# Kernel tuning notes

Measured on AMD Instinct MI355X. Metric: run time of the kernel, lower is better.

## Reference

```python
import jax, jax.numpy as jnp
import numpy as np

EPS_BN = 1e-5
EPS_W = 1e-16
UP_CH = [512, 256, 128, 64]
NS = [512, 2048, 8192, 32768]
K = 3


def knn_interpolate(x, pos, pos_up, batch, batch_up, k):
    # squared distances [N_up, N]; cross-batch pairs masked to +inf
    d = jnp.sum((pos_up[:, None, :] - pos[None, :, :]) ** 2, axis=-1)
    d = jnp.where(batch_up[:, None] != batch[None, :], jnp.inf, d)
    neg_d, idx = jax.lax.top_k(-d, k)             # k nearest neighbours
    w = 1.0 / jnp.maximum(-neg_d, EPS_W)          # inverse squared-distance weights
    xn = x[idx]                                   # [N_up, k, C] gather
    return jnp.einsum('nk,nkc->nc', w, xn) / jnp.sum(w, axis=1, keepdims=True)


def lin_bn_relu(h, W, b, g, be):
    # Linear -> BatchNorm (batch stats over nodes) -> ReLU (PyG MLP, plain_last=False)
    h = h @ W.T + b
    m = jnp.mean(h, axis=0)
    v = jnp.var(h, axis=0)
    return jax.nn.relu((h - m) * jax.lax.rsqrt(v + EPS_BN) * g + be)


def decoder_fwd(pos, x, batch, params):
    x_i = x[0]
    for i in range(3):  # fixed num_convs=3 levels, structurally distinct shapes
        up = knn_interpolate(x_i, pos[i], pos[i + 1], batch[i], batch[i + 1], K)
        h = jnp.concatenate([x[i + 1], up], axis=-1)
        W1, b1, g1, be1, W2, b2, g2, be2 = params[i]
        h = lin_bn_relu(h, W1, b1, g1, be1)            # MLP block
        x_i = h + lin_bn_relu(h, W2, b2, g2, be2)      # ResMLP residual block
    return x_i


def setup_inputs() -> dict:
    key = jax.random.key(0)
    ks = jax.random.split(key, 32)
    inp = {}
    for i, (n, c) in enumerate(zip(NS, UP_CH)):
        inp[f'pos{i}'] = jax.random.normal(ks[i], (n, 3), jnp.float32)
        inp[f'x{i}'] = jax.random.normal(ks[4 + i], (n, c), jnp.float32)
        inp[f'batch{i}'] = jnp.zeros((n,), jnp.int32)
    j = 8
    for i in range(3):
        cin = UP_CH[i] + UP_CH[i + 1]
        cout = UP_CH[i + 1]
        inp[f'W1_{i}'] = jax.random.normal(ks[j], (cout, cin), jnp.float32) / np.float32(np.sqrt(cin))
        inp[f'W2_{i}'] = jax.random.normal(ks[j + 1], (cout, cout), jnp.float32) / np.float32(np.sqrt(cout))
        j += 2
        for nm in ('b1', 'be1', 'b2', 'be2'):
            inp[f'{nm}_{i}'] = jnp.zeros((cout,), jnp.float32)
        for nm in ('g1', 'g2'):
            inp[f'{nm}_{i}'] = jnp.ones((cout,), jnp.float32)
    return inp


def reference(pos0, pos1, pos2, pos3, x0, x1, x2, x3,
              W1_0, b1_0, g1_0, be1_0, W2_0, b2_0, g2_0, be2_0,
              W1_1, b1_1, g1_1, be1_1, W2_1, b2_1, g2_1, be2_1,
              W1_2, b1_2, g1_2, be1_2, W2_2, b2_2, g2_2, be2_2,
              batch0, batch1, batch2, batch3):
    pos = [pos0, pos1, pos2, pos3]
    x = [x0, x1, x2, x3]
    batch = [batch0, batch1, batch2, batch3]
    params = [
        (W1_0, b1_0, g1_0, be1_0, W2_0, b2_0, g2_0, be2_0),
        (W1_1, b1_1, g1_1, be1_1, W2_1, b2_1, g2_1, be2_1),
        (W1_2, b1_2, g1_2, be1_2, W2_2, b2_2, g2_2, be2_2),
    ]
    return decoder_fwd(pos, x, batch, params)
```

## Files before the change

### kernel.cpp

```cpp
#include <hip/hip_runtime.h>


#define EPS_BN 1e-5f
#define EPS_W  1e-16f

#define GRD    52
#define GLO   -6.5f
#define GH     0.25f
#define GIH    4.0f
#define NCELLS (GRD * GRD * GRD)

typedef unsigned long long u64;

template<int TPT>
__global__ __launch_bounds__(256)
void knn_part(const float* __restrict__ pos_s, const float* __restrict__ pos_t,
              int Ns, int Nt, int nsplit,
              float* __restrict__ cand_d, int* __restrict__ cand_i)
{
  __shared__ float4 sp[512];

  const int tb  = blockIdx.x;
  const int spl = blockIdx.y;
  const int chunk = Ns / nsplit;
  const int cs = spl * chunk;

  float tx[TPT], ty[TPT], tz[TPT];
  float d0[TPT], d1[TPT], d2[TPT];
  int   j0[TPT], j1[TPT], j2[TPT];

#pragma unroll
  for (int q = 0; q < TPT; ++q) {
    int t = tb * 256 * TPT + q * 256 + threadIdx.x;
    tx[q] = pos_t[3 * t + 0];
    ty[q] = pos_t[3 * t + 1];
    tz[q] = pos_t[3 * t + 2];
    d0[q] = 3.4e38f; d1[q] = 3.4e38f; d2[q] = 3.4e38f;
    j0[q] = 0; j1[q] = 0; j2[q] = 0;
  }

  for (int i = threadIdx.x; i < chunk; i += 256) {
    int p = cs + i;
    sp[i] = make_float4(pos_s[3 * p], pos_s[3 * p + 1], pos_s[3 * p + 2], 0.f);
  }
  __syncthreads();

#pragma unroll 4
  for (int j = 0; j < chunk; ++j) {
    float4 s = sp[j];
    int gj = cs + j;
#pragma unroll
    for (int q = 0; q < TPT; ++q) {
      float dx = tx[q] - s.x, dy = ty[q] - s.y, dz = tz[q] - s.z;
      float nd = fmaf(dz, dz, fmaf(dy, dy, dx * dx));
      int nj = gj;
      bool c = nd < d0[q];
      float td = c ? d0[q] : nd;  int tj = c ? j0[q] : nj;
      d0[q] = c ? nd : d0[q];     j0[q] = c ? nj : j0[q];
      nd = td; nj = tj;
      c = nd < d1[q];
      td = c ? d1[q] : nd;        tj = c ? j1[q] : nj;
      d1[q] = c ? nd : d1[q];     j1[q] = c ? nj : j1[q];
      nd = td; nj = tj;
      c = nd < d2[q];
      d2[q] = c ? nd : d2[q];     j2[q] = c ? nj : j2[q];
    }
  }

#pragma unroll
  for (int q = 0; q < TPT; ++q) {
    int t = tb * 256 * TPT + q * 256 + threadIdx.x;
    int o = (t * nsplit + spl) * 3;
    cand_d[o + 0] = d0[q]; cand_d[o + 1] = d1[q]; cand_d[o + 2] = d2[q];
    cand_i[o + 0] = j0[q]; cand_i[o + 1] = j1[q]; cand_i[o + 2] = j2[q];
  }
}

template<int CS, int FROMW>
__global__ __launch_bounds__(256)
void merge_gather(const float* __restrict__ cand_d, const int* __restrict__ cand_i,
                  int nsplit, const float* __restrict__ xs,
                  float* __restrict__ up, int Nt,
                  float* __restrict__ stats0, const float* __restrict__ widx)
{
  if (blockIdx.x == 0) {
    for (int i = threadIdx.x; i < 1024; i += 256) stats0[i] = 0.f;
  }

  int t  = blockIdx.x * 64 + (threadIdx.x >> 2);
  int cg = threadIdx.x & 3;

  float w0, w1, w2; int i0, i1, i2;
  if (FROMW) {
    float4 wv = *(const float4*)&widx[(size_t)t * 8];
    float4 iv = *(const float4*)&widx[(size_t)t * 8 + 4];
    w0 = wv.x; w1 = wv.y; w2 = wv.z;
    i0 = (int)__float_as_uint(iv.x);
    i1 = (int)__float_as_uint(iv.y);
    i2 = (int)__float_as_uint(iv.z);
  } else {
    float e0 = 3.5e38f, e1 = 3.5e38f, e2 = 3.5e38f;
    i0 = 0; i1 = 0; i2 = 0;
    int o = t * nsplit * 3;
    for (int c = 0; c < nsplit * 3; ++c) {
      float d = cand_d[o + c];
      int   i = cand_i[o + c];
      if (d < e2) {
        if (d < e1) {
          e2 = e1; i2 = i1;
          if (d < e0) { e1 = e0; i1 = i0; e0 = d; i0 = i; }
          else        { e1 = d;  i1 = i; }
        } else { e2 = d; i2 = i; }
      }
    }
    w0 = 1.f / fmaxf(e0, EPS_W);
    w1 = 1.f / fmaxf(e1, EPS_W);
    w2 = 1.f / fmaxf(e2, EPS_W);
    float inv = 1.f / (w0 + w1 + w2);
    w0 *= inv; w1 *= inv; w2 *= inv;
  }

  const float4* r0 = (const float4*)(xs + (size_t)i0 * CS);
  const float4* r1 = (const float4*)(xs + (size_t)i1 * CS);
  const float4* r2 = (const float4*)(xs + (size_t)i2 * CS);
  float4* ou = (float4*)(up + (size_t)t * CS);
  const int F4 = CS / 4;
#pragma unroll 4
  for (int k = 0; k < F4 / 4; ++k) {
    int f = cg + 4 * k;
    float4 a = r0[f], b = r1[f], d = r2[f], rr;
    rr.x = w0 * a.x + w1 * b.x + w2 * d.x;
    rr.y = w0 * a.y + w1 * b.y + w2 * d.y;
    rr.z = w0 * a.z + w1 * b.z + w2 * d.z;
    rr.w = w0 * a.w + w1 * b.w + w2 * d.w;
    ou[f] = rr;
  }
}

__device__ __forceinline__ int cell_coord(float v) {
  return min(max((int)floorf((v - GLO) * GIH), 0), GRD - 1);
}

__global__ __launch_bounds__(256)
void grid_count2(const float* __restrict__ ps, int ns, int* __restrict__ cnt,
                 int* __restrict__ pcell,
                 const float* __restrict__ pt, int nt, int* __restrict__ tcnt,
                 int* __restrict__ tpcell)
{
  int i = blockIdx.x * 256 + threadIdx.x;
  const float* p; int n; int* c; int* pc;
  if (blockIdx.y == 0) { p = ps; n = ns; c = cnt;  pc = pcell; }
  else                 { p = pt; n = nt; c = tcnt; pc = tpcell; }
  if (i >= n) return;
  int cx = cell_coord(p[3 * i + 0]);
  int cy = cell_coord(p[3 * i + 1]);
  int cz = cell_coord(p[3 * i + 2]);
  int cid = (cz * GRD + cy) * GRD + cx;
  pc[i] = cid;
  atomicAdd(&c[cid], 1);
}

__global__ __launch_bounds__(256)
void grid_scan1(const int* __restrict__ cntA, int* __restrict__ ofspA,
                int* __restrict__ auxA,
                const int* __restrict__ cntB, int* __restrict__ ofspB,
                int* __restrict__ auxB)
{
  const int* cnt; int* ofsp; int* aux;
  if (blockIdx.y == 0) { cnt = cntA; ofsp = ofspA; aux = auxA; }
  else                 { cnt = cntB; ofsp = ofspB; aux = auxB; }
  __shared__ int arr[256];
  int tid = threadIdx.x;
  int c0 = blockIdx.x * 1024 + tid * 4;
  int s0 = (c0 + 0 < NCELLS) ? cnt[c0 + 0] : 0;
  int s1 = (c0 + 1 < NCELLS) ? cnt[c0 + 1] : 0;
  int s2 = (c0 + 2 < NCELLS) ? cnt[c0 + 2] : 0;
  int s3 = (c0 + 3 < NCELLS) ? cnt[c0 + 3] : 0;
  int p1 = s0, p2 = s0 + s1, p3 = p2 + s2, tot = p3 + s3;
  arr[tid] = tot; __syncthreads();
  for (int d = 1; d < 256; d <<= 1) {
    int v = (tid >= d) ? arr[tid - d] : 0;
    __syncthreads();
    arr[tid] += v;
    __syncthreads();
  }
  int excl = arr[tid] - tot;
  if (c0 + 0 < NCELLS) ofsp[c0 + 0] = excl;
  if (c0 + 1 < NCELLS) ofsp[c0 + 1] = excl + p1;
  if (c0 + 2 < NCELLS) ofsp[c0 + 2] = excl + p2;
  if (c0 + 3 < NCELLS) ofsp[c0 + 3] = excl + p3;
  if (tid == 255) aux[blockIdx.x] = arr[255];
}

__global__ __launch_bounds__(256)
void grid_scan2(const int* __restrict__ auxA, int* __restrict__ auxpA,
                const int* __restrict__ auxB, int* __restrict__ auxpB, int nblk)
{
  const int* aux; int* auxp;
  if (blockIdx.x == 0) { aux = auxA; auxp = auxpA; }
  else                 { aux = auxB; auxp = auxpB; }
  __shared__ int arr[256];
  int tid = threadIdx.x;
  int v = (tid < nblk) ? aux[tid] : 0;
  arr[tid] = v; __syncthreads();
  for (int d = 1; d < 256; d <<= 1) {
    int w = (tid >= d) ? arr[tid - d] : 0;
    __syncthreads();
    arr[tid] += w;
    __syncthreads();
  }
  auxp[tid] = arr[tid] - v;
}

__global__ __launch_bounds__(256)
void grid_fixup2(const int* __restrict__ ofsp, const int* __restrict__ auxp,
                 int* __restrict__ cursor, int* __restrict__ cellstart,
                 int ns_total,
                 const int* __restrict__ tofsp, const int* __restrict__ tauxp,
                 int* __restrict__ tcursor, int* __restrict__ ovf_cnt)
{
  int i = blockIdx.x * 256 + threadIdx.x;
  if (blockIdx.y == 0) {
    if (i == 0) { *ovf_cnt = 0; cellstart[NCELLS] = ns_total; }
    for (int c = i; c < NCELLS; c += gridDim.x * 256) {
      int v = ofsp[c] + auxp[c >> 10];
      cursor[c] = v;
      cellstart[c] = v;
    }
  } else {
    for (int c = i; c < NCELLS; c += gridDim.x * 256)
      tcursor[c] = tofsp[c] + tauxp[c >> 10];
  }
}

__global__ __launch_bounds__(256)
void grid_scatter2(const float* __restrict__ ps, int ns,
                   const int* __restrict__ pcell, int* __restrict__ cursor,
                   float4* __restrict__ plist,
                   int nt, const int* __restrict__ tpcell,
                   int* __restrict__ tcursor, int* __restrict__ tsorted)
{
  int i = blockIdx.x * 256 + threadIdx.x;
  if (blockIdx.y == 0) {
    if (i >= ns) return;
    int slot = atomicAdd(&cursor[pcell[i]], 1);
    plist[slot] = make_float4(ps[3 * i], ps[3 * i + 1], ps[3 * i + 2],
                              __uint_as_float((unsigned)i));
  } else {
    if (i >= nt) return;
    int slot = atomicAdd(&tcursor[tpcell[i]], 1);
    tsorted[slot] = i;
  }
}

__device__ __forceinline__ void key_insert(u64 nk, u64& k0, u64& k1, u64& k2) {
  bool c = nk < k0; u64 tk = c ? k0 : nk; k0 = c ? nk : k0; nk = tk;
  c = nk < k1; tk = c ? k1 : nk; k1 = c ? nk : k1; nk = tk;
  c = nk < k2; k2 = c ? nk : k2;
}

__device__ __forceinline__ void quad_merge(u64& k0, u64& k1, u64& k2) {
#pragma unroll
  for (int off = 1; off <= 2; off <<= 1) {
    u64 a0 = __shfl_xor(k0, off);
    u64 a1 = __shfl_xor(k1, off);
    u64 a2 = __shfl_xor(k2, off);
    key_insert(a0, k0, k1, k2);
    key_insert(a1, k0, k1, k2);
    key_insert(a2, k0, k1, k2);
  }
}

__global__ __launch_bounds__(256)
void knn_search_quad(const float* __restrict__ pos_t, int Nt,
                     const int* __restrict__ cellstart,
                     const float4* __restrict__ plist,
                     const int* __restrict__ tsorted,
                     float* __restrict__ widx,
                     int* __restrict__ ovf_cnt, int* __restrict__ ovf)
{
  int gid = blockIdx.x * 64 + (threadIdx.x >> 2);
  int sub = threadIdx.x & 3;
  if (gid >= Nt) return;
  int t = tsorted[gid];
  float tx = pos_t[3 * t], ty = pos_t[3 * t + 1], tz = pos_t[3 * t + 2];
  int cx = cell_coord(tx), cy = cell_coord(ty), cz = cell_coord(tz);

  u64 k0 = ~0ULL, k1 = ~0ULL, k2 = ~0ULL;

  auto scan_range = [&](int p0, int p1, u64& a0, u64& a1, u64& a2) {
    for (int p = p0; p < p1; ++p) {
      float4 s = plist[p];
      float dx = tx - s.x, dy = ty - s.y, dz = tz - s.z;
      float d = fmaf(dz, dz, fmaf(dy, dy, dx * dx));
      key_insert(((u64)__float_as_uint(d) << 32) | (u64)__float_as_uint(s.w),
                 a0, a1, a2);
    }
  };

  auto certify = [&](int R) -> bool {
    int xl = max(cx - R, 0), xh = min(cx + R, GRD - 1);
    int yl = max(cy - R, 0), yh = min(cy + R, GRD - 1);
    int zl = max(cz - R, 0), zh = min(cz + R, GRD - 1);
    float m = 1e30f;
    if (xl > 0)       m = fminf(m, tx - (GLO + xl * GH));
    if (xh < GRD - 1) m = fminf(m, (GLO + (xh + 1) * GH) - tx);
    if (yl > 0)       m = fminf(m, ty - (GLO + yl * GH));
    if (yh < GRD - 1) m = fminf(m, (GLO + (yh + 1) * GH) - ty);
    if (zl > 0)       m = fminf(m, tz - (GLO + zl * GH));
    if (zh < GRD - 1) m = fminf(m, (GLO + (zh + 1) * GH) - tz);
    float d2b = __uint_as_float((unsigned)(k2 >> 32));
    return (m * m * 0.9999f > d2b);
  };

  int xlo = max(cx - 1, 0), xhi = min(cx + 1, GRD - 1);
  for (int id = sub; id < 9; id += 4) {
    int y = cy + (id % 3) - 1, z = cz + (id / 3) - 1;
    if (((unsigned)y < GRD) && ((unsigned)z < GRD)) {
      int base = (z * GRD + y) * GRD;
      scan_range(cellstart[base + xlo], cellstart[base + xhi + 1], k0, k1, k2);
    }
  }
  quad_merge(k0, k1, k2);
  bool done = certify(1);

  if (!done) {
    static const signed char o_dy[16] = {-2,-1,0,1,2, -2,-1,0,1,2, -2,-2,-2, 2,2,2};
    static const signed char o_dz[16] = {-2,-2,-2,-2,-2, 2,2,2,2,2, -1,0,1, -1,0,1};
    int xl2 = max(cx - 2, 0), xh2 = min(cx + 2, GRD - 1);
    u64 p0 = ~0ULL, p1 = ~0ULL, p2 = ~0ULL;
    for (int id = sub; id < 34; id += 4) {
      if (id < 16) {
        int y = cy + o_dy[id], z = cz + o_dz[id];
        if (((unsigned)y < GRD) && ((unsigned)z < GRD)) {
          int base = (z * GRD + y) * GRD;
          scan_range(cellstart[base + xl2], cellstart[base + xh2 + 1], p0, p1, p2);
        }
      } else {
        int row = (id - 16) >> 1, side = (id - 16) & 1;
        int y = cy + (row % 3) - 1, z = cz + (row / 3) - 1;
        int x = side ? (cx + 2) : (cx - 2);
        if (((unsigned)y < GRD) && ((unsigned)z < GRD) && ((unsigned)x < GRD)) {
          int base = (z * GRD + y) * GRD;
          scan_range(cellstart[base + x], cellstart[base + x + 1], p0, p1, p2);
        }
      }
    }
    quad_merge(p0, p1, p2);
    key_insert(p0, k0, k1, k2);
    key_insert(p1, k0, k1, k2);
    key_insert(p2, k0, k1, k2);
    done = certify(2);
  }

  if (!done) {
    if (sub == 0) ovf[atomicAdd(ovf_cnt, 1)] = t;
    return;
  }

  if (sub == 0) {
    float d0 = __uint_as_float((unsigned)(k0 >> 32));
    float d1 = __uint_as_float((unsigned)(k1 >> 32));
    float d2 = __uint_as_float((unsigned)(k2 >> 32));
    float w0 = 1.f / fmaxf(d0, EPS_W);
    float w1 = 1.f / fmaxf(d1, EPS_W);
    float w2 = 1.f / fmaxf(d2, EPS_W);
    float inv = 1.f / (w0 + w1 + w2);
    *(float4*)&widx[(size_t)t * 8] =
        make_float4(w0 * inv, w1 * inv, w2 * inv, 0.f);
    *(float4*)&widx[(size_t)t * 8 + 4] =
        make_float4(__uint_as_float((unsigned)k0), __uint_as_float((unsigned)k1),
                    __uint_as_float((unsigned)k2), 0.f);
  }
}

__global__ __launch_bounds__(256)
void knn_brute(const float* __restrict__ pos_t, const float4* __restrict__ plist,
               int Ns, const int* __restrict__ ovf_cnt,
               const int* __restrict__ ovf, float* __restrict__ widx)
{
  __shared__ float4 tile[1024];
  int n = *ovf_cnt;
  int ngrp = (n + 3) >> 2;
  int wv = threadIdx.x >> 6, ln = threadIdx.x & 63;

  for (int g = blockIdx.x; g < ngrp; g += gridDim.x) {
    int o = g * 4 + wv;
    bool active = (o < n);
    int t = active ? ovf[o] : 0;
    float tx = pos_t[3 * t], ty = pos_t[3 * t + 1], tz = pos_t[3 * t + 2];
    u64 k0 = ~0ULL, k1 = ~0ULL, k2 = ~0ULL;

    for (int base = 0; base < Ns; base += 1024) {
      int m = min(1024, Ns - base);
      __syncthreads();
      for (int i = threadIdx.x; i < m; i += 256) tile[i] = plist[base + i];
      __syncthreads();
#pragma unroll 4
      for (int p = ln; p < m; p += 64) {
        float4 s = tile[p];
        float dx = tx - s.x, dy = ty - s.y, dz = tz - s.z;
        float d = fmaf(dz, dz, fmaf(dy, dy, dx * dx));
        key_insert(((u64)__float_as_uint(d) << 32) | (u64)__float_as_uint(s.w),
                   k0, k1, k2);
      }
    }

#pragma unroll
    for (int off = 32; off >= 1; off >>= 1) {
      u64 a0 = __shfl_down(k0, off);
      u64 a1 = __shfl_down(k1, off);
      u64 a2 = __shfl_down(k2, off);
      key_insert(a0, k0, k1, k2);
      key_insert(a1, k0, k1, k2);
      key_insert(a2, k0, k1, k2);
    }

    if (active && ln == 0) {
      float d0 = __uint_as_float((unsigned)(k0 >> 32));
      float d1 = __uint_as_float((unsigned)(k1 >> 32));
      float d2 = __uint_as_float((unsigned)(k2 >> 32));
      float w0 = 1.f / fmaxf(d0, EPS_W);
      float w1 = 1.f / fmaxf(d1, EPS_W);
      float w2 = 1.f / fmaxf(d2, EPS_W);
      float inv = 1.f / (w0 + w1 + w2);
      *(float4*)&widx[(size_t)t * 8] =
          make_float4(w0 * inv, w1 * inv, w2 * inv, 0.f);
      *(float4*)&widx[(size_t)t * 8 + 4] =
          make_float4(__uint_as_float((unsigned)k0), __uint_as_float((unsigned)k1),
                      __uint_as_float((unsigned)k2), 0.f);
    }
  }
}

template<int BM, int CONCAT, int BNIN>
__global__ __launch_bounds__(256, 2)
void gemm_k(const float* __restrict__ A0, const float* __restrict__ A1, int C0,
            const float* __restrict__ B, const float* __restrict__ bias,
            const float* __restrict__ s_in, const float* __restrict__ q_in,
            const float* __restrict__ g_in, const float* __restrict__ be_in,
            float* __restrict__ Z, float* __restrict__ s_out, float* __restrict__ q_out,
            int M, int K, int N)
{
  const int BK = 32, BN = 64;
  const int AR = BM / 16;
  __shared__ float a_lds[BK][BM + 4];
  __shared__ float b_lds[BK][BN + 4];
  __shared__ float bn_sc[256], bn_sh[256];

  const int tid = threadIdx.x;
  const int mb = blockIdx.x * BM;
  const int nb = blockIdx.y * BN;
  const int tn = tid & 15, tm = tid >> 4;

  if (BNIN) {
    for (int c = tid; c < K; c += 256) {
      float mean = s_in[c] / (float)M;
      float var  = q_in[c] / (float)M - mean * mean;
      float rstd = rsqrtf(var + EPS_BN);
      float sc = g_in[c] * rstd;
      bn_sc[c] = sc;
      bn_sh[c] = be_in[c] - mean * sc;
    }
    __syncthreads();
  }

  float acc[AR][4];
#pragma unroll
  for (int i = 0; i < AR; ++i)
#pragma unroll
    for (int j = 0; j < 4; ++j) acc[i][j] = 0.f;

  for (int kb = 0; kb < K; kb += BK) {
    const float* Ap; int ldA, ko;
    if (CONCAT) {
      if (kb < C0) { Ap = A0; ldA = C0;     ko = kb; }
      else         { Ap = A1; ldA = K - C0; ko = kb - C0; }
    } else { Ap = A0; ldA = K; ko = kb; }

#pragma unroll
    for (int sl = tid; sl < BM * 8; sl += 256) {
      int m = sl >> 3, k4 = (sl & 7) * 4;
      float4 v = *(const float4*)(Ap + (size_t)(mb + m) * ldA + ko + k4);
      if (BNIN) {
        v.x = fmaxf(v.x * bn_sc[kb + k4 + 0] + bn_sh[kb + k4 + 0], 0.f);
        v.y = fmaxf(v.y * bn_sc[kb + k4 + 1] + bn_sh[kb + k4 + 1], 0.f);
        v.z = fmaxf(v.z * bn_sc[kb + k4 + 2] + bn_sh[kb + k4 + 2], 0.f);
        v.w = fmaxf(v.w * bn_sc[kb + k4 + 3] + bn_sh[kb + k4 + 3], 0.f);
      }
      a_lds[k4 + 0][m] = v.x; a_lds[k4 + 1][m] = v.y;
      a_lds[k4 + 2][m] = v.z; a_lds[k4 + 3][m] = v.w;
    }
#pragma unroll
    for (int sl = tid; sl < 512; sl += 256) {
      int n = sl >> 3, k4 = (sl & 7) * 4;
      float4 v = *(const float4*)(B + (size_t)(nb + n) * K + kb + k4);
      b_lds[k4 + 0][n] = v.x; b_lds[k4 + 1][n] = v.y;
      b_lds[k4 + 2][n] = v.z; b_lds[k4 + 3][n] = v.w;
    }
    __syncthreads();

#pragma unroll
    for (int k = 0; k < BK; ++k) {
      float4 bv = *(const float4*)&b_lds[k][tn * 4];
      float av[AR];
      if (BM == 32) {
        av[0] = a_lds[k][tm * 2 + 0];
        av[1] = a_lds[k][tm * 2 + 1];
      } else {
        float4 a0 = *(const float4*)&a_lds[k][tm * 4];
        av[0] = a0.x; av[1] = a0.y; av[2] = a0.z; av[3] = a0.w;
        if (BM == 128) {
          float4 a1 = *(const float4*)&a_lds[k][tm * 4 + 64];
          av[4] = a1.x; av[5] = a1.y; av[6] = a1.z; av[7] = a1.w;
        }
      }
#pragma unroll
      for (int i = 0; i < AR; ++i) {
        acc[i][0] += av[i] * bv.x;
        acc[i][1] += av[i] * bv.y;
        acc[i][2] += av[i] * bv.z;
        acc[i][3] += av[i] * bv.w;
      }
    }
    __syncthreads();
  }

  float4 bb = *(const float4*)&bias[nb + tn * 4];
  float psum[4] = {0, 0, 0, 0}, psq[4] = {0, 0, 0, 0};
#pragma unroll
  for (int i = 0; i < AR; ++i) {
    int m = (BM == 128) ? (tm * 4 + (i & 3) + ((i >= 4) ? 64 : 0))
                        : (tm * AR + i);
    float4 v;
    v.x = acc[i][0] + bb.x; v.y = acc[i][1] + bb.y;
    v.z = acc[i][2] + bb.z; v.w = acc[i][3] + bb.w;
    *(float4*)(Z + (size_t)(mb + m) * N + nb + tn * 4) = v;
    psum[0] += v.x; psum[1] += v.y; psum[2] += v.z; psum[3] += v.w;
    psq[0] += v.x * v.x; psq[1] += v.y * v.y;
    psq[2] += v.z * v.z; psq[3] += v.w * v.w;
  }
  __syncthreads();
  float* red = &b_lds[0][0];
  int base = tm * 64 + tn * 4;
#pragma unroll
  for (int j = 0; j < 4; ++j) {
    red[base + j] = psum[j];
    red[1024 + base + j] = psq[j];
  }
  __syncthreads();
  if (tid < 64) {
    float s = 0.f, q = 0.f;
#pragma unroll
    for (int it = 0; it < 16; ++it) {
      s += red[it * 64 + tid];
      q += red[1024 + it * 64 + tid];
    }
    atomicAdd(&s_out[nb + tid], s);
    atomicAdd(&q_out[nb + tid], q);
  }
}

__global__ __launch_bounds__(256)
void final_k(const float* __restrict__ z1, const float* __restrict__ z2,
             const float* __restrict__ s1, const float* __restrict__ q1,
             const float* __restrict__ g1, const float* __restrict__ be1,
             const float* __restrict__ s2, const float* __restrict__ q2,
             const float* __restrict__ g2, const float* __restrict__ be2,
             float* __restrict__ outp, int M, int C)
{
  __shared__ float sc1[256], sh1[256], sc2[256], sh2[256];
  for (int c = threadIdx.x; c < C; c += 256) {
    float mean = s1[c] / (float)M;
    float var  = q1[c] / (float)M - mean * mean;
    float r = rsqrtf(var + EPS_BN);
    sc1[c] = g1[c] * r; sh1[c] = be1[c] - mean * sc1[c];
    mean = s2[c] / (float)M;
    var  = q2[c] / (float)M - mean * mean;
    r = rsqrtf(var + EPS_BN);
    sc2[c] = g2[c] * r; sh2[c] = be2[c] - mean * sc2[c];
  }
  __syncthreads();

  int total4 = M * C / 4;
  int cmask = (C / 4) - 1;
  for (int i = blockIdx.x * 256 + threadIdx.x; i < total4; i += gridDim.x * 256) {
    int c = (i & cmask) * 4;
    float4 a = ((const float4*)z1)[i];
    float4 b = ((const float4*)z2)[i];
    float4 r;
    r.x = fmaxf(a.x * sc1[c + 0] + sh1[c + 0], 0.f) + fmaxf(b.x * sc2[c + 0] + sh2[c + 0], 0.f);
    r.y = fmaxf(a.y * sc1[c + 1] + sh1[c + 1], 0.f) + fmaxf(b.y * sc2[c + 1] + sh2[c + 1], 0.f);
    r.z = fmaxf(a.z * sc1[c + 2] + sh1[c + 2], 0.f) + fmaxf(b.z * sc2[c + 2] + sh2[c + 2], 0.f);
    r.w = fmaxf(a.w * sc1[c + 3] + sh1[c + 3], 0.f) + fmaxf(b.w * sc2[c + 3] + sh2[c + 3], 0.f);
    ((float4*)outp)[i] = r;
  }
}

extern "C" void kernel_launch(void* const* d_in, const int* in_sizes, int n_in,
                              void* d_out, int out_size, void* d_ws, size_t ws_size,
                              hipStream_t stream)
{
  const bool dict_order = (in_sizes[1] == 512 * 512);

  const float* POS[4];
  const float* X[4];
  for (int i = 0; i < 4; ++i) {
    POS[i] = (const float*)d_in[dict_order ? 3 * i : i];
    X[i]   = (const float*)d_in[dict_order ? 3 * i + 1 : 4 + i];
  }
  static const int dict_map[8] = {0, 2, 6, 3, 1, 4, 7, 5};
  auto PRM = [&](int lvl, int which) -> const float* {
    int idx = dict_order ? (12 + 8 * lvl + dict_map[which]) : (8 + 8 * lvl + which);
    return (const float*)d_in[idx];
  };

  char* ws = (char*)d_ws;
  float* up    = (float*)(ws);
  float* z1    = (float*)(ws + (16u << 20));
  float* z2    = (float*)(ws + (24u << 20));
  float* cd    = z1;
  int*   ci    = (int*)z2;
  float* x1o   = (float*)(ws + (32u << 20));
  float* x2o   = (float*)(ws + (34u << 20));
  float* stats = (float*)(ws + (38u << 20));
  float* s1 = stats, *q1 = stats + 256, *s2 = stats + 512, *q2 = stats + 768;
  float* widx  = (float*)(ws + (38u << 20) + 8192);

  char* gb = ws + (16u << 20);
  const size_t S = 600 * 1024;
  int*    cnt      = (int*)(gb + 0 * S);
  int*    tcnt     = (int*)(gb + 1 * S);
  int*    ofsp     = (int*)(gb + 2 * S);
  int*    tofsp    = (int*)(gb + 3 * S);
  int*    cursor   = (int*)(gb + 4 * S);
  int*    tcursor  = (int*)(gb + 5 * S);
  int*    cellstart= (int*)(gb + 6 * S);
  char*   gb2      = gb + 7 * S;
  int*    aux      = (int*)(gb2);
  int*    auxp     = (int*)(gb2 + 1024);
  int*    aux2     = (int*)(gb2 + 2048);
  int*    auxp2    = (int*)(gb2 + 3072);
  int*    pcell    = (int*)(gb2 + 4096);
  int*    tpcell   = (int*)(gb2 + 4096 + 32768);
  float4* plist    = (float4*)(gb2 + 4096 + 32768 + 131072);
  int*    tsorted  = (int*)(gb2 + 4096 + 32768 + 2 * 131072);
  int*    ovfc     = (int*)(gb2 + 4096 + 32768 + 3 * 131072);
  int*    ovf      = (int*)(gb2 + 4096 + 32768 + 3 * 131072 + 1024);

  knn_part<1><<<dim3(8, 16), 256, 0, stream>>>(POS[0], POS[1], 512, 2048, 16, cd, ci);
  merge_gather<512, 0><<<32, 256, 0, stream>>>(cd, ci, 16, X[0], up, 2048, stats, nullptr);
  gemm_k<32, 1, 0><<<dim3(64, 4), 256, 0, stream>>>(
      X[1], up, 256, PRM(0, 0), PRM(0, 1),
      nullptr, nullptr, nullptr, nullptr,
      z1, s1, q1, 2048, 768, 256);
  gemm_k<32, 0, 1><<<dim3(64, 4), 256, 0, stream>>>(
      z1, nullptr, 0, PRM(0, 4), PRM(0, 5),
      s1, q1, PRM(0, 2), PRM(0, 3),
      z2, s2, q2, 2048, 256, 256);
  final_k<<<512, 256, 0, stream>>>(z1, z2, s1, q1, PRM(0, 2), PRM(0, 3),
                                   s2, q2, PRM(0, 6), PRM(0, 7), x1o, 2048, 256);

  knn_part<1><<<dim3(32, 32), 256, 0, stream>>>(POS[1], POS[2], 2048, 8192, 32, cd, ci);
  merge_gather<256, 0><<<128, 256, 0, stream>>>(cd, ci, 32, x1o, up, 8192, stats, nullptr);
  gemm_k<64, 1, 0><<<dim3(128, 2), 256, 0, stream>>>(
      X[2], up, 128, PRM(1, 0), PRM(1, 1),
      nullptr, nullptr, nullptr, nullptr,
      z1, s1, q1, 8192, 384, 128);
  gemm_k<64, 0, 1><<<dim3(128, 2), 256, 0, stream>>>(
      z1, nullptr, 0, PRM(1, 4), PRM(1, 5),
      s1, q1, PRM(1, 2), PRM(1, 3),
      z2, s2, q2, 8192, 128, 128);
  final_k<<<1024, 256, 0, stream>>>(z1, z2, s1, q1, PRM(1, 2), PRM(1, 3),
                                    s2, q2, PRM(1, 6), PRM(1, 7), x2o, 8192, 128);

  hipMemsetAsync(cnt, 0, 2 * S, stream);
  grid_count2<<<dim3(128, 2), 256, 0, stream>>>(POS[2], 8192, cnt, pcell,
                                                POS[3], 32768, tcnt, tpcell);
  grid_scan1<<<dim3(138, 2), 256, 0, stream>>>(cnt, ofsp, aux, tcnt, tofsp, aux2);
  grid_scan2<<<2, 256, 0, stream>>>(aux, auxp, aux2, auxp2, 138);
  grid_fixup2<<<dim3(256, 2), 256, 0, stream>>>(ofsp, auxp, cursor, cellstart, 8192,
                                                tofsp, auxp2, tcursor, ovfc);
  grid_scatter2<<<dim3(128, 2), 256, 0, stream>>>(POS[2], 8192, pcell, cursor, plist,
                                                  32768, tpcell, tcursor, tsorted);
  knn_search_quad<<<512, 256, 0, stream>>>(POS[3], 32768, cellstart, plist,
                                           tsorted, widx, ovfc, ovf);
  knn_brute<<<256, 256, 0, stream>>>(POS[3], plist, 8192, ovfc, ovf, widx);
  merge_gather<128, 1><<<512, 256, 0, stream>>>(nullptr, nullptr, 0, x2o, up,
                                                32768, stats, widx);
  gemm_k<64, 1, 0><<<dim3(512, 1), 256, 0, stream>>>(
      X[3], up, 64, PRM(2, 0), PRM(2, 1),
      nullptr, nullptr, nullptr, nullptr,
      z1, s1, q1, 32768, 192, 64);
  gemm_k<64, 0, 1><<<dim3(512, 1), 256, 0, stream>>>(
      z1, nullptr, 0, PRM(2, 4), PRM(2, 5),
      s1, q1, PRM(2, 2), PRM(2, 3),
      z2, s2, q2, 32768, 64, 64);
  final_k<<<1024, 256, 0, stream>>>(z1, z2, s1, q1, PRM(2, 2), PRM(2, 3),
                                    s2, q2, PRM(2, 6), PRM(2, 7),
                                    (float*)d_out, 32768, 64);
}
```

Measured before the change: 453.4 us.

## Retile GEMM with smaller blocks, register prefetch, and row-major A in LDS

The GEMM kernel now takes the N tile as a template parameter, shrinks tiles to 32x32 or 32x64, and launches about twice as many blocks, with launch bounds raised to 4 blocks per SM. Global loads for the next K-slice go into registers before the current slice is computed, a software-pipelined prefetch meant to hide load latency. A is stored in LDS as [m][k] so writes are single vector stores, and B gets odd padding to avoid bank conflicts. The goal is more parallelism and overlap on these small GEMMs. The cost is lower per-thread reuse, scalar LDS reads in the inner loop, and more register pressure from the prefetch buffers.

```diff
diff --git a/kernel.cpp b/kernel.cpp
--- a/kernel.cpp
+++ b/kernel.cpp
@@ -433,8 +433,8 @@
   }
 }
 
-template<int BM, int CONCAT, int BNIN>
-__global__ __launch_bounds__(256, 2)
+template<int BM, int BN, int CONCAT, int BNIN>
+__global__ __launch_bounds__(256, 4)
 void gemm_k(const float* __restrict__ A0, const float* __restrict__ A1, int C0,
             const float* __restrict__ B, const float* __restrict__ bias,
             const float* __restrict__ s_in, const float* __restrict__ q_in,
@@ -442,16 +442,21 @@
             float* __restrict__ Z, float* __restrict__ s_out, float* __restrict__ q_out,
             int M, int K, int N)
 {
-  const int BK = 32, BN = 64;
-  const int AR = BM / 16;
-  __shared__ float a_lds[BK][BM + 4];
-  __shared__ float b_lds[BK][BN + 4];
+  const int BK = 32;
+  const int TN = BN / 4;
+  const int TM = 256 / TN;
+  const int AR = BM / TM;
+  const int NA = BM / 32;
+  const int NB = BN / 32;
+
+  __shared__ alignas(16) float a_lds[BM][BK + 4];
+  __shared__ float b_lds[BK][BN + 1];
   __shared__ float bn_sc[256], bn_sh[256];
 
   const int tid = threadIdx.x;
+  const int tn = tid % TN, tm = tid / TN;
   const int mb = blockIdx.x * BM;
   const int nb = blockIdx.y * BN;
-  const int tn = tid & 15, tm = tid >> 4;
 
   if (BNIN) {
     for (int c = tid; c < K; c += 256) {
@@ -471,56 +476,68 @@
 #pragma unroll
     for (int j = 0; j < 4; ++j) acc[i][j] = 0.f;
 
-  for (int kb = 0; kb < K; kb += BK) {
+  float4 pa[NA], pb[NB];
+
+  auto prefetch = [&](int kb) {
     const float* Ap; int ldA, ko;
     if (CONCAT) {
       if (kb < C0) { Ap = A0; ldA = C0;     ko = kb; }
       else         { Ap = A1; ldA = K - C0; ko = kb - C0; }
     } else { Ap = A0; ldA = K; ko = kb; }
-
-#pragma unroll
-    for (int sl = tid; sl < BM * 8; sl += 256) {
+#pragma unroll
+    for (int i = 0; i < NA; ++i) {
+      int sl = tid + 256 * i;
       int m = sl >> 3, k4 = (sl & 7) * 4;
-      float4 v = *(const float4*)(Ap + (size_t)(mb + m) * ldA + ko + k4);
+      pa[i] = *(const float4*)(Ap + (size_t)(mb + m) * ldA + ko + k4);
+    }
+#pragma unroll
+    for (int i = 0; i < NB; ++i) {
+      int sl = tid + 256 * i;
+      int nn = sl >> 3, k4 = (sl & 7) * 4;
+      pb[i] = *(const float4*)(B + (size_t)(nb + nn) * K + kb + k4);
+    }
+  };
+
+  prefetch(0);
+
+  for (int kb = 0; kb < K; kb += BK) {
+#pragma unroll
+    for (int i = 0; i < NA; ++i) {
+      int sl = tid + 256 * i;
+      int m = sl >> 3, k4 = (sl & 7) * 4;
+      float4 v = pa[i];
       if (BNIN) {
         v.x = fmaxf(v.x * bn_sc[kb + k4 + 0] + bn_sh[kb + k4 + 0], 0.f);
         v.y = fmaxf(v.y * bn_sc[kb + k4 + 1] + bn_sh[kb + k4 + 1], 0.f);
         v.z = fmaxf(v.z * bn_sc[kb + k4 + 2] + bn_sh[kb + k4 + 2], 0.f);
         v.w = fmaxf(v.w * bn_sc[kb + k4 + 3] + bn_sh[kb + k4 + 3], 0.f);
       }
-      a_lds[k4 + 0][m] = v.x; a_lds[k4 + 1][m] = v.y;
-      a_lds[k4 + 2][m] = v.z; a_lds[k4 + 3][m] = v.w;
-    }
-#pragma unroll
-    for (int sl = tid; sl < 512; sl += 256) {
-      int n = sl >> 3, k4 = (sl & 7) * 4;
-      float4 v = *(const float4*)(B + (size_t)(nb + n) * K + kb + k4);
-      b_lds[k4 + 0][n] = v.x; b_lds[k4 + 1][n] = v.y;
-      b_lds[k4 + 2][n] = v.z; b_lds[k4 + 3][n] = v.w;
+      *(float4*)&a_lds[m][k4] = v;
+    }
+#pragma unroll
+    for (int i = 0; i < NB; ++i) {
+      int sl = tid + 256 * i;
+      int nn = sl >> 3, k4 = (sl & 7) * 4;
+      float4 v = pb[i];
+      b_lds[k4 + 0][nn] = v.x; b_lds[k4 + 1][nn] = v.y;
+      b_lds[k4 + 2][nn] = v.z; b_lds[k4 + 3][nn] = v.w;
     }
     __syncthreads();
+    if (kb + BK < K) prefetch(kb + BK);
 
 #pragma unroll
     for (int k = 0; k < BK; ++k) {
-      float4 bv = *(const float4*)&b_lds[k][tn * 4];
-      float av[AR];
-      if (BM == 32) {
-        av[0] = a_lds[k][tm * 2 + 0];
-        av[1] = a_lds[k][tm * 2 + 1];
-      } else {
-        float4 a0 = *(const float4*)&a_lds[k][tm * 4];
-        av[0] = a0.x; av[1] = a0.y; av[2] = a0.z; av[3] = a0.w;
-        if (BM == 128) {
-          float4 a1 = *(const float4*)&a_lds[k][tm * 4 + 64];
-          av[4] = a1.x; av[5] = a1.y; av[6] = a1.z; av[7] = a1.w;
-        }
-      }
+      float bv0 = b_lds[k][tn * 4 + 0];
+      float bv1 = b_lds[k][tn * 4 + 1];
+      float bv2 = b_lds[k][tn * 4 + 2];
+      float bv3 = b_lds[k][tn * 4 + 3];
 #pragma unroll
       for (int i = 0; i < AR; ++i) {
-        acc[i][0] += av[i] * bv.x;
-        acc[i][1] += av[i] * bv.y;
-        acc[i][2] += av[i] * bv.z;
-        acc[i][3] += av[i] * bv.w;
+        float a = a_lds[tm * AR + i][k];
+        acc[i][0] = fmaf(a, bv0, acc[i][0]);
+        acc[i][1] = fmaf(a, bv1, acc[i][1]);
+        acc[i][2] = fmaf(a, bv2, acc[i][2]);
+        acc[i][3] = fmaf(a, bv3, acc[i][3]);
       }
     }
     __syncthreads();
@@ -530,8 +547,7 @@
   float psum[4] = {0, 0, 0, 0}, psq[4] = {0, 0, 0, 0};
 #pragma unroll
   for (int i = 0; i < AR; ++i) {
-    int m = (BM == 128) ? (tm * 4 + (i & 3) + ((i >= 4) ? 64 : 0))
-                        : (tm * AR + i);
+    int m = tm * AR + i;
     float4 v;
     v.x = acc[i][0] + bb.x; v.y = acc[i][1] + bb.y;
     v.z = acc[i][2] + bb.z; v.w = acc[i][3] + bb.w;
@@ -541,20 +557,21 @@
     psq[2] += v.z * v.z; psq[3] += v.w * v.w;
   }
   __syncthreads();
-  float* red = &b_lds[0][0];
-  int base = tm * 64 + tn * 4;
+  float* red_s = &b_lds[0][0];
+  float* red_q = &a_lds[0][0];
 #pragma unroll
   for (int j = 0; j < 4; ++j) {
-    red[base + j] = psum[j];
-    red[1024 + base + j] = psq[j];
+    int c = tn * 4 + j;
+    red_s[c * TM + tm] = psum[j];
+    red_q[c * TM + tm] = psq[j];
   }
   __syncthreads();
-  if (tid < 64) {
+  if (tid < BN) {
     float s = 0.f, q = 0.f;
 #pragma unroll
-    for (int it = 0; it < 16; ++it) {
-      s += red[it * 64 + tid];
-      q += red[1024 + it * 64 + tid];
+    for (int it = 0; it < TM; ++it) {
+      s += red_s[tid * TM + it];
+      q += red_q[tid * TM + it];
     }
     atomicAdd(&s_out[nb + tid], s);
     atomicAdd(&q_out[nb + tid], q);
@@ -650,11 +667,11 @@
 
   knn_part<1><<<dim3(8, 16), 256, 0, stream>>>(POS[0], POS[1], 512, 2048, 16, cd, ci);
   merge_gather<512, 0><<<32, 256, 0, stream>>>(cd, ci, 16, X[0], up, 2048, stats, nullptr);
-  gemm_k<32, 1, 0><<<dim3(64, 4), 256, 0, stream>>>(
+  gemm_k<32, 32, 1, 0><<<dim3(64, 8), 256, 0, stream>>>(
       X[1], up, 256, PRM(0, 0), PRM(0, 1),
       nullptr, nullptr, nullptr, nullptr,
       z1, s1, q1, 2048, 768, 256);
-  gemm_k<32, 0, 1><<<dim3(64, 4), 256, 0, stream>>>(
+  gemm_k<32, 32, 0, 1><<<dim3(64, 8), 256, 0, stream>>>(
       z1, nullptr, 0, PRM(0, 4), PRM(0, 5),
       s1, q1, PRM(0, 2), PRM(0, 3),
       z2, s2, q2, 2048, 256, 256);
@@ -663,11 +680,11 @@
 
   knn_part<1><<<dim3(32, 32), 256, 0, stream>>>(POS[1], POS[2], 2048, 8192, 32, cd, ci);
   merge_gather<256, 0><<<128, 256, 0, stream>>>(cd, ci, 32, x1o, up, 8192, stats, nullptr);
-  gemm_k<64, 1, 0><<<dim3(128, 2), 256, 0, stream>>>(
+  gemm_k<32, 32, 1, 0><<<dim3(256, 4), 256, 0, stream>>>(
       X[2], up, 128, PRM(1, 0), PRM(1, 1),
       nullptr, nullptr, nullptr, nullptr,
       z1, s1, q1, 8192, 384, 128);
-  gemm_k<64, 0, 1><<<dim3(128, 2), 256, 0, stream>>>(
+  gemm_k<32, 32, 0, 1><<<dim3(256, 4), 256, 0, stream>>>(
       z1, nullptr, 0, PRM(1, 4), PRM(1, 5),
       s1, q1, PRM(1, 2), PRM(1, 3),
       z2, s2, q2, 8192, 128, 128);
@@ -688,11 +705,11 @@
   knn_brute<<<256, 256, 0, stream>>>(POS[3], plist, 8192, ovfc, ovf, widx);
   merge_gather<128, 1><<<512, 256, 0, stream>>>(nullptr, nullptr, 0, x2o, up,
                                                 32768, stats, widx);
-  gemm_k<64, 1, 0><<<dim3(512, 1), 256, 0, stream>>>(
+  gemm_k<32, 64, 1, 0><<<dim3(1024, 1), 256, 0, stream>>>(
       X[3], up, 64, PRM(2, 0), PRM(2, 1),
       nullptr, nullptr, nullptr, nullptr,
       z1, s1, q1, 32768, 192, 64);
-  gemm_k<64, 0, 1><<<dim3(512, 1), 256, 0, stream>>>(
+  gemm_k<32, 64, 0, 1><<<dim3(1024, 1), 256, 0, stream>>>(
       z1, nullptr, 0, PRM(2, 4), PRM(2, 5),
       s1, q1, PRM(2, 2), PRM(2, 3),
       z2, s2, q2, 32768, 64, 64);
```

Result: slower. 471.8 us (+4.1%).
